# Kernel optimization log

Hardware: AMD Instinct MI355X
Metric: run time of the kernel (lower is better)

Reference implementation:

```python
import jax, jax.numpy as jnp
import numpy as np

D_MODEL = 1024
N_HEADS = 16
D_FF = 4096
D_K = D_MODEL // N_HEADS


def _ln(x, g, b, eps=1e-5):
    mu = jnp.mean(x, axis=-1, keepdims=True)
    var = jnp.mean(jnp.square(x - mu), axis=-1, keepdims=True)
    return (x - mu) * jax.lax.rsqrt(var + eps) * g + b


def setup_inputs() -> dict:
    key = jax.random.key(0)
    ks = jax.random.split(key, 16)
    s = 0.02
    inp = {
        "x": jax.random.normal(ks[0], (2, 2048, D_MODEL), dtype=jnp.float32),
        "Wq": jax.random.normal(ks[1], (D_MODEL, D_MODEL), dtype=jnp.float32) * s,
        "bq": jnp.zeros((D_MODEL,), jnp.float32),
        "Wk": jax.random.normal(ks[2], (D_MODEL, D_MODEL), dtype=jnp.float32) * s,
        "bk": jnp.zeros((D_MODEL,), jnp.float32),
        "Wv": jax.random.normal(ks[3], (D_MODEL, D_MODEL), dtype=jnp.float32) * s,
        "bv": jnp.zeros((D_MODEL,), jnp.float32),
        "Wo": jax.random.normal(ks[4], (D_MODEL, D_MODEL), dtype=jnp.float32) * s,
        "bo": jnp.zeros((D_MODEL,), jnp.float32),
        "W1": jax.random.normal(ks[5], (D_MODEL, D_FF), dtype=jnp.float32) * s,
        "b1": jnp.zeros((D_FF,), jnp.float32),
        "W2": jax.random.normal(ks[6], (D_FF, D_MODEL), dtype=jnp.float32) * s,
        "b2": jnp.zeros((D_MODEL,), jnp.float32),
        "g1": jnp.ones((D_MODEL,), jnp.float32),
        "be1": jnp.zeros((D_MODEL,), jnp.float32),
        "g2": jnp.ones((D_MODEL,), jnp.float32),
        "be2": jnp.zeros((D_MODEL,), jnp.float32),
    }
    return inp


def reference(x, Wq, bq, Wk, bk, Wv, bv, Wo, bo, W1, b1, W2, b2, g1, be1, g2, be2):
    B, L, D = x.shape
    # QKV projections -> [B, H, L, d_k]
    q = (x @ Wq + bq).reshape(B, L, N_HEADS, D_K).transpose(0, 2, 1, 3)
    k = (x @ Wk + bk).reshape(B, L, N_HEADS, D_K).transpose(0, 2, 1, 3)
    v = (x @ Wv + bv).reshape(B, L, N_HEADS, D_K).transpose(0, 2, 1, 3)
    scores = jnp.einsum("bhqd,bhkd->bhqk", q, k) / jnp.sqrt(jnp.float32(D_K))
    attn = jax.nn.softmax(scores, axis=-1)
    ctx = jnp.einsum("bhqk,bhkd->bhqd", attn, v)
    ctx = ctx.transpose(0, 2, 1, 3).reshape(B, L, D)
    attn_out = ctx @ Wo + bo
    # residual + LN1
    h = _ln(x + attn_out, g1, be1)
    # FFN (exact GELU, matching torch F.gelu default)
    ff = jax.nn.gelu(h @ W1 + b1, approximate=False) @ W2 + b2
    return _ln(h + ff, g2, be2)
```

## Files before the change

### kernel.cpp

```cpp
#include <hip/hip_runtime.h>
#include <cmath>


typedef unsigned short u16;
typedef unsigned int u32;
typedef __attribute__((ext_vector_type(8))) __bf16 bf16x8;
typedef __attribute__((ext_vector_type(4))) float f32x4;

#define MFMA16(a, b, c) __builtin_amdgcn_mfma_f32_16x16x32_bf16(a, b, c, 0, 0, 0)

__device__ __forceinline__ u16 f2bf(float f) {
  u32 u = __builtin_bit_cast(u32, f);
  u += 0x7fffu + ((u >> 16) & 1u);
  return (u16)(u >> 16);
}

__device__ __forceinline__ u32 packtrunc(float lo, float hi) {
#if __has_builtin(__builtin_amdgcn_perm)
  return __builtin_amdgcn_perm(__builtin_bit_cast(u32, hi),
                               __builtin_bit_cast(u32, lo), 0x07060302u);
#else
  return (__builtin_bit_cast(u32, lo) >> 16) |
         (__builtin_bit_cast(u32, hi) & 0xFFFF0000u);
#endif
}

__device__ __forceinline__ bf16x8 ld_frag(const u16* p) {
  return __builtin_bit_cast(bf16x8, *(const uint4*)p);
}

__device__ __forceinline__ float fexp2(float x) {
#if __has_builtin(__builtin_amdgcn_exp2f)
  return __builtin_amdgcn_exp2f(x);
#else
  return exp2f(x);
#endif
}

__device__ __forceinline__ float frcp(float x) {
#if __has_builtin(__builtin_amdgcn_rcpf)
  return __builtin_amdgcn_rcpf(x);
#else
  return 1.0f / x;
#endif
}

__device__ __forceinline__ float gelu_f(float v) {
  float x = v * 0.70710678118654752f;
  float a = fabsf(x);
  float t = frcp(fmaf(0.3275911f, a, 1.0f));
  float p = fmaf(1.061405429f, t, -1.453152027f);
  p = fmaf(p, t, 1.421413741f);
  p = fmaf(p, t, -0.284496736f);
  p = fmaf(p, t, 0.254829592f);
  p = p * t;
  float e = fexp2(-a * a * 1.4426950408889634f);
  float er = copysignf(1.0f - p * e, x);
  return 0.5f * v * (1.0f + er);
}

__device__ __forceinline__ void gload16(const u16* g, u16* l) {
  __builtin_amdgcn_global_load_lds(
      (const __attribute__((address_space(1))) void*)g,
      (__attribute__((address_space(3))) void*)l, 16, 0, 0);
}

#define WAITVL(N) asm volatile("s_waitcnt vmcnt(" #N ") lgkmcnt(0)" ::: "memory")
#define BAR() do { __builtin_amdgcn_s_barrier(); asm volatile("" ::: "memory"); } while (0)

__global__ __launch_bounds__(256) void cvt_bf16_k(const float* __restrict__ src,
                                                  u16* __restrict__ dst) {
  int i = (blockIdx.x * 256 + threadIdx.x) * 4;
  float4 v = *(const float4*)(src + i);
  ushort4 o;
  o.x = f2bf(v.x); o.y = f2bf(v.y); o.z = f2bf(v.z); o.w = f2bf(v.w);
  *(ushort4*)(dst + i) = o;
}

__global__ __launch_bounds__(256) void transpose_bf16_k(const float* __restrict__ src,
                                                        u16* __restrict__ dst,
                                                        int R, int C) {
  __shared__ float tile[32][33];
  int tx = threadIdx.x & 31, ty = threadIdx.x >> 5;
  int c0 = blockIdx.x * 32, r0 = blockIdx.y * 32;
#pragma unroll
  for (int i = 0; i < 4; i++)
    tile[ty + 8 * i][tx] = src[(long)(r0 + ty + 8 * i) * C + c0 + tx];
  __syncthreads();
#pragma unroll
  for (int i = 0; i < 4; i++)
    dst[(long)(c0 + ty + 8 * i) * R + r0 + tx] = f2bf(tile[tx][ty + 8 * i]);
}

__global__ __launch_bounds__(256) void transpose4_bf16_k(
    const float* __restrict__ Wq, const float* __restrict__ Wk,
    const float* __restrict__ Wv, const float* __restrict__ Wo,
    u16* __restrict__ wqkvT, u16* __restrict__ woT) {
  const int z = blockIdx.z;
  const float* src = (z == 0) ? Wq : (z == 1) ? Wk : (z == 2) ? Wv : Wo;
  u16* dst = (z < 3) ? (wqkvT + (size_t)z * 1024 * 1024) : woT;
  __shared__ float tile[32][33];
  int tx = threadIdx.x & 31, ty = threadIdx.x >> 5;
  int c0 = blockIdx.x * 32, r0 = blockIdx.y * 32;
#pragma unroll
  for (int i = 0; i < 4; i++)
    tile[ty + 8 * i][tx] = src[(long)(r0 + ty + 8 * i) * 1024 + c0 + tx];
  __syncthreads();
#pragma unroll
  for (int i = 0; i < 4; i++)
    dst[(long)(c0 + ty + 8 * i) * 1024 + r0 + tx] = f2bf(tile[tx][ty + 8 * i]);
}

template <int MODE>
__global__ __launch_bounds__(256, 3) void gemm128_k(
    const u16* __restrict__ A, const u16* __restrict__ BT,
    int N, int lda, int ldb, int Kc,
    const float* __restrict__ bias, float* __restrict__ outF,
    u16* __restrict__ outB, float* __restrict__ p1,
    u16* __restrict__ qd, u16* __restrict__ kd, u16* __restrict__ vTd,
    const float* __restrict__ bq, const float* __restrict__ bk,
    const float* __restrict__ bv) {
  __shared__ u16 As[3][128 * 32];
  __shared__ u16 Bs[3][128 * 32];
  const int tid = threadIdx.x;
  const int wave = tid >> 6, lane = tid & 63, quad = lane >> 4, l16 = lane & 15;
  const int wm = wave >> 1, wn = wave & 1;
  const int gx = gridDim.x;
  int flat = blockIdx.y * gx + blockIdx.x;
  const int cpx = (gx * gridDim.y) >> 3;
  flat = (flat & 7) * cpx + (flat >> 3);
  const int m0 = (flat / gx) * 128, n0 = (flat % gx) * 128;
  const int kz = blockIdx.z;
  const long kofs = (long)kz * Kc;
  const int KT = Kc >> 5;

  const int srow = lane >> 2;
  const int sseg = (lane & 3) ^ (srow & 3);
  const u16* aS = A + (long)(m0 + wave * 32 + srow) * lda + kofs + sseg * 8;
  const u16* bS = BT + (long)(n0 + wave * 32 + srow) * ldb + kofs + sseg * 8;

  auto stage = [&](int sb, int s) {
    const u16* pa = aS + (long)s * 32;
    gload16(pa, &As[sb][wave * 1024]);
    gload16(pa + 16 * (long)lda, &As[sb][wave * 1024 + 512]);
    const u16* pb = bS + (long)s * 32;
    gload16(pb, &Bs[sb][wave * 1024]);
    gload16(pb + 16 * (long)ldb, &Bs[sb][wave * 1024 + 512]);
  };

  int aro[4], bro[4];
#pragma unroll
  for (int f = 0; f < 4; f++) {
    int ra = wm * 64 + f * 16 + l16;
    aro[f] = ra * 32 + ((quad ^ (ra & 3)) * 8);
    int rb = wn * 64 + f * 16 + l16;
    bro[f] = rb * 32 + ((quad ^ (rb & 3)) * 8);
  }

  f32x4 acc[4][4] = {};

  stage(0, 0);
  stage(1, 1);
  int buf = 0;
#pragma unroll 1
  for (int t = 0; t < KT; ++t) {
    if (t < KT - 1) { WAITVL(4); } else { WAITVL(0); }
    BAR();
    bf16x8 af[4], bfr[4];
#pragma unroll
    for (int i = 0; i < 4; i++) af[i] = ld_frag(&As[buf][aro[i]]);
#pragma unroll
    for (int i = 0; i < 4; i++) bfr[i] = ld_frag(&Bs[buf][bro[i]]);
    if (t + 2 < KT) {
      int nb = buf + 2; if (nb >= 3) nb -= 3;
      stage(nb, t + 2);
    }
    __builtin_amdgcn_s_setprio(1);
#pragma unroll
    for (int mf = 0; mf < 4; mf++)
#pragma unroll
      for (int nf = 0; nf < 4; nf++)
        acc[mf][nf] = MFMA16(af[mf], bfr[nf], acc[mf][nf]);
    __builtin_amdgcn_s_setprio(0);
    if (++buf == 3) buf = 0;
  }

  if (MODE == 0) {
    const int nbase = n0 + wn * 64;
    const int mat = nbase >> 10;
    const float* bp = (mat == 0) ? bq : ((mat == 1) ? bk : bv);
    float bb[4];
    int hh0[4], dd0[4];
#pragma unroll
    for (int nf = 0; nf < 4; nf++) {
      int nn = (nbase + nf * 16 + l16) & 1023;
      bb[nf] = bp[nn];
      hh0[nf] = nn >> 6;
      dd0[nf] = nn & 63;
    }
    if (mat < 2) {
#pragma unroll
      for (int mf = 0; mf < 4; mf++) {
#pragma unroll
        for (int r = 0; r < 4; r++) {
          int mr = m0 + wm * 64 + mf * 16 + quad * 4 + r;
          int bI = mr >> 11, ll = mr & 2047;
#pragma unroll
          for (int nf = 0; nf < 4; nf++) {
            float v = acc[mf][nf][r] + bb[nf];
            long idx = ((long)((bI * 16 + hh0[nf]) * 2048 + ll)) * 64 + dd0[nf];
            if (mat == 0) {
              qd[idx] = f2bf(v * 0.18033688011112043f);
            } else {
              kd[idx] = f2bf(v);
            }
          }
        }
      }
    } else {
#pragma unroll
      for (int nf = 0; nf < 4; nf++) {
#pragma unroll
        for (int mf = 0; mf < 4; mf++) {
#pragma unroll
          for (int r = 0; r < 4; r++) {
            int mr = m0 + wm * 64 + mf * 16 + quad * 4 + r;
            int bI = mr >> 11, ll = mr & 2047;
            float v = acc[mf][nf][r] + bb[nf];
            vTd[((long)((bI * 16 + hh0[nf]) * 64 + dd0[nf])) * 2048 + ll] = f2bf(v);
          }
        }
      }
    }
  } else if (MODE == 2) {
    float bb[4];
#pragma unroll
    for (int nf = 0; nf < 4; nf++) bb[nf] = bias[n0 + wn * 64 + nf * 16 + l16];
#pragma unroll
    for (int mf = 0; mf < 4; mf++) {
#pragma unroll
      for (int r = 0; r < 4; r++) {
        int mr = m0 + wm * 64 + mf * 16 + quad * 4 + r;
        u16* orow = outB + (long)mr * N + n0 + wn * 64 + l16;
#pragma unroll
        for (int nf = 0; nf < 4; nf++)
          orow[nf * 16] = f2bf(gelu_f(acc[mf][nf][r] + bb[nf]));
      }
    }
  } else {
    float* sl = (kz == 0) ? outF : p1;
#pragma unroll
    for (int mf = 0; mf < 4; mf++) {
#pragma unroll
      for (int r = 0; r < 4; r++) {
        int mr = m0 + wm * 64 + mf * 16 + quad * 4 + r;
        float* orow = sl + (long)mr * N + n0 + wn * 64 + l16;
#pragma unroll
        for (int nf = 0; nf < 4; nf++) orow[nf * 16] = acc[mf][nf][r];
      }
    }
  }
}

template <int MODE, int TN>
__global__ __launch_bounds__(256) void gemm_k(
    const u16* __restrict__ A, const u16* __restrict__ BT, int M, int N, int K,
    const float* __restrict__ bias, float* __restrict__ outF) {
  constexpr int NT = TN / 32;
  __shared__ u16 As[2][128 * 32];
  __shared__ u16 Bs[2][TN * 32];
  const int tid = threadIdx.x;
  const int wave = tid >> 6, lane = tid & 63, quad = lane >> 4, l16 = lane & 15;
  const int wm = wave >> 1, wn = wave & 1;
  const int m0 = blockIdx.y * 128, n0 = blockIdx.x * TN;

  const int srow = lane >> 2;
  const int sxor = (lane & 3) ^ (srow & 3);
  const u16* aS0 = A + (long)(m0 + wave * 32 + srow) * K + sxor * 8;
  const u16* aS1 = aS0 + 16 * K;
  const u16* bS0 = BT + (long)(n0 + (TN == 128 ? wave * 32 : wave * 16) + srow) * K + sxor * 8;
  const u16* bS1 = bS0 + 16 * K;

  int aoff[4], boff[NT];
#pragma unroll
  for (int t = 0; t < 4; t++) {
    int ra = wm * 64 + t * 16 + l16;
    aoff[t] = ra * 32 + ((quad ^ (l16 & 3)) * 8);
  }
#pragma unroll
  for (int t = 0; t < NT; t++) {
    int rb = wn * (TN / 2) + t * 16 + l16;
    boff[t] = rb * 32 + ((quad ^ (l16 & 3)) * 8);
  }

  auto stage = [&](int buf, int k0) {
    gload16(aS0 + k0, &As[buf][(wave * 2 + 0) * 512]);
    gload16(aS1 + k0, &As[buf][(wave * 2 + 1) * 512]);
    if (TN == 128) {
      gload16(bS0 + k0, &Bs[buf][(wave * 2 + 0) * 512]);
      gload16(bS1 + k0, &Bs[buf][(wave * 2 + 1) * 512]);
    } else {
      gload16(bS0 + k0, &Bs[buf][wave * 512]);
    }
  };

  f32x4 acc[4][NT] = {};

  stage(0, 0);
#pragma unroll 1
  for (int k0 = 0; k0 < K; k0 += 32) {
    const int buf = (k0 >> 5) & 1;
    __syncthreads();
    if (k0 + 32 < K) stage(buf ^ 1, k0 + 32);
    bf16x8 af[4], bfr[NT];
#pragma unroll
    for (int t = 0; t < 4; t++) af[t] = ld_frag(&As[buf][aoff[t]]);
#pragma unroll
    for (int t = 0; t < NT; t++) bfr[t] = ld_frag(&Bs[buf][boff[t]]);
#pragma unroll
    for (int mt = 0; mt < 4; mt++)
#pragma unroll
      for (int nt = 0; nt < NT; nt++)
        acc[mt][nt] = MFMA16(af[mt], bfr[nt], acc[mt][nt]);
  }

  if (MODE == 1) {
    float bb[NT];
#pragma unroll
    for (int nt = 0; nt < NT; nt++) bb[nt] = bias[n0 + wn * (TN / 2) + nt * 16 + l16];
#pragma unroll
    for (int mt = 0; mt < 4; mt++) {
#pragma unroll
      for (int r = 0; r < 4; r++) {
        int mr = m0 + wm * 64 + mt * 16 + quad * 4 + r;
        float* orow = outF + (long)mr * N + n0 + wn * (TN / 2) + l16;
#pragma unroll
        for (int nt = 0; nt < NT; nt++)
          orow[nt * 16] = acc[mt][nt][r] + bb[nt];
      }
    }
  }
}

__global__ __launch_bounds__(256, 3) void attn_k(const u16* __restrict__ qd,
                                                 const u16* __restrict__ kd,
                                                 const u16* __restrict__ vTd,
                                                 u16* __restrict__ ctx) {
  __shared__ u16 Ks[2][64 * 64];
  __shared__ u16 Vs[2][64 * 64];
  __shared__ __align__(16) u16 P[4][32][72];
  const int tid = threadIdx.x;
  const int wave = tid >> 6, lane = tid & 63, quad = lane >> 4, l16 = lane & 15;
  const int bh = blockIdx.y;
  const u16* Q = qd + (long)bh * 2048 * 64;
  const u16* Kp = kd + (long)bh * 2048 * 64;
  const u16* Vt = vTd + (long)bh * 64 * 2048;
  const int qbase = blockIdx.x * 128 + wave * 32;

  bf16x8 qf[2][2];
#pragma unroll
  for (int qs = 0; qs < 2; qs++) {
    qf[qs][0] = ld_frag(Q + (qbase + qs * 16 + l16) * 64 + quad * 8);
    qf[qs][1] = ld_frag(Q + (qbase + qs * 16 + l16) * 64 + 32 + quad * 8);
  }

  f32x4 o[2][4] = {};
  float m[2] = {-1e30f, -1e30f}, l[2] = {0.f, 0.f};

  const int srow = lane >> 3;
  const int sx = (lane & 7) ^ srow;
  const int kr0 = wave * 16 + srow;
  const int kr1 = wave * 16 + 8 + srow;

  const int fs0 = ((0 * 4 + quad) ^ (l16 & 7)) * 8;
  const int fs1 = ((1 * 4 + quad) ^ (l16 & 7)) * 8;

  auto stage = [&](int buf, int j0) {
    gload16(Kp + (long)(j0 + kr0) * 64 + sx * 8, &Ks[buf][(wave * 2 + 0) * 512]);
    gload16(Kp + (long)(j0 + kr1) * 64 + sx * 8, &Ks[buf][(wave * 2 + 1) * 512]);
    gload16(Vt + (long)kr0 * 2048 + j0 + sx * 8, &Vs[buf][(wave * 2 + 0) * 512]);
    gload16(Vt + (long)kr1 * 2048 + j0 + sx * 8, &Vs[buf][(wave * 2 + 1) * 512]);
  };

  stage(0, 0);

#pragma unroll 1
  for (int j0 = 0; j0 < 2048; j0 += 64) {
    const int buf = (j0 >> 6) & 1;
    __syncthreads();
    if (j0 + 64 < 2048) stage(buf ^ 1, j0 + 64);

    const u16* kb = &Ks[buf][0];
    f32x4 st[2][4];
#pragma unroll
    for (int f = 0; f < 4; f++) {
      bf16x8 k0 = ld_frag(kb + (f * 16 + l16) * 64 + fs0);
      bf16x8 k1 = ld_frag(kb + (f * 16 + l16) * 64 + fs1);
      f32x4 s0 = {}, s1 = {};
      s0 = MFMA16(k0, qf[0][0], s0); s0 = MFMA16(k1, qf[0][1], s0);
      s1 = MFMA16(k0, qf[1][0], s1); s1 = MFMA16(k1, qf[1][1], s1);
      st[0][f] = s0; st[1][f] = s1;
    }

#pragma unroll
    for (int qs = 0; qs < 2; qs++) {
      float mx = -1e30f;
#pragma unroll
      for (int f = 0; f < 4; f++)
        mx = fmaxf(mx, fmaxf(fmaxf(st[qs][f][0], st[qs][f][1]),
                             fmaxf(st[qs][f][2], st[qs][f][3])));
      mx = fmaxf(mx, __shfl_xor(mx, 16));
      mx = fmaxf(mx, __shfl_xor(mx, 32));
      if (__any(mx > m[qs] + 8.0f)) {
        float mn = fmaxf(m[qs], mx);
        float al = fexp2(m[qs] - mn);
        m[qs] = mn;
        l[qs] *= al;
#pragma unroll
        for (int nt = 0; nt < 4; nt++) {
          o[qs][nt][0] *= al; o[qs][nt][1] *= al;
          o[qs][nt][2] *= al; o[qs][nt][3] *= al;
        }
      }
      float sm = 0.f;
      u16* prow = &P[wave][qs * 16 + l16][0];
#pragma unroll
      for (int f = 0; f < 4; f++) {
        float p0 = fexp2(st[qs][f][0] - m[qs]);
        float p1 = fexp2(st[qs][f][1] - m[qs]);
        float p2 = fexp2(st[qs][f][2] - m[qs]);
        float p3 = fexp2(st[qs][f][3] - m[qs]);
        sm += (p0 + p1) + (p2 + p3);
        uint2 u;
        u.x = packtrunc(p0, p1);
        u.y = packtrunc(p2, p3);
        *(uint2*)(prow + f * 16 + quad * 4) = u;
      }
      sm += __shfl_xor(sm, 16);
      sm += __shfl_xor(sm, 32);
      l[qs] += sm;
    }
    __asm__ volatile("s_waitcnt lgkmcnt(0)" ::: "memory");

    const u16* vb = &Vs[buf][0];
    bf16x8 vf[4][2];
#pragma unroll
    for (int nt = 0; nt < 4; nt++) {
      vf[nt][0] = ld_frag(vb + (nt * 16 + l16) * 64 + fs0);
      vf[nt][1] = ld_frag(vb + (nt * 16 + l16) * 64 + fs1);
    }
#pragma unroll
    for (int qs = 0; qs < 2; qs++) {
      const u16* prow = &P[wave][qs * 16 + l16][0];
#pragma unroll
      for (int kh = 0; kh < 2; kh++) {
        bf16x8 pf = ld_frag(prow + kh * 32 + quad * 8);
#pragma unroll
        for (int nt = 0; nt < 4; nt++)
          o[qs][nt] = MFMA16(vf[nt][kh], pf, o[qs][nt]);
      }
    }
  }

  const int bI = bh >> 4, hh = bh & 15;
#pragma unroll
  for (int qs = 0; qs < 2; qs++) {
    const float rl = 1.0f / l[qs];
    const long row = (long)(bI * 2048 + qbase + qs * 16 + l16);
#pragma unroll
    for (int nt = 0; nt < 4; nt++) {
      ushort4 w;
      w.x = f2bf(o[qs][nt][0] * rl);
      w.y = f2bf(o[qs][nt][1] * rl);
      w.z = f2bf(o[qs][nt][2] * rl);
      w.w = f2bf(o[qs][nt][3] * rl);
      *(ushort4*)(ctx + row * 1024 + hh * 64 + nt * 16 + quad * 4) = w;
    }
  }
}

__global__ __launch_bounds__(256) void ln_k(const float* __restrict__ a,
                                            const float* __restrict__ b,
                                            const float* __restrict__ g,
                                            const float* __restrict__ be,
                                            float* __restrict__ outF,
                                            u16* __restrict__ outB) {
  const int row = blockIdx.x, tid = threadIdx.x;
  const float* pa = a + (long)row * 1024;
  const float* pb = b + (long)row * 1024;
  float v[4], s = 0.f, sq = 0.f;
#pragma unroll
  for (int i = 0; i < 4; i++) {
    int c = i * 256 + tid;
    v[i] = pa[c] + pb[c];
    s += v[i];
    sq += v[i] * v[i];
  }
#pragma unroll
  for (int off = 1; off < 64; off <<= 1) {
    s += __shfl_xor(s, off);
    sq += __shfl_xor(sq, off);
  }
  __shared__ float red[10];
  int wave = tid >> 6, lane = tid & 63;
  if (lane == 0) { red[wave * 2] = s; red[wave * 2 + 1] = sq; }
  __syncthreads();
  if (tid == 0) {
    float S = red[0] + red[2] + red[4] + red[6];
    float Q = red[1] + red[3] + red[5] + red[7];
    float mu = S * (1.0f / 1024.0f);
    float var = Q * (1.0f / 1024.0f) - mu * mu;
    red[8] = mu;
    red[9] = rsqrtf(var + 1e-5f);
  }
  __syncthreads();
  float mu = red[8], rstd = red[9];
#pragma unroll
  for (int i = 0; i < 4; i++) {
    int c = i * 256 + tid;
    float o = (v[i] - mu) * rstd * g[c] + be[c];
    outF[(long)row * 1024 + c] = o;
    if (outB) outB[(long)row * 1024 + c] = f2bf(o);
  }
}

__global__ __launch_bounds__(256) void ln2s_k(const float* __restrict__ a,
                                              const float* __restrict__ q0,
                                              const float* __restrict__ q1,
                                              const float* __restrict__ bias,
                                              const float* __restrict__ g,
                                              const float* __restrict__ be,
                                              float* __restrict__ outF) {
  const int row = blockIdx.x, tid = threadIdx.x;
  const long base = (long)row * 1024;
  float v[4], s = 0.f, sq = 0.f;
#pragma unroll
  for (int i = 0; i < 4; i++) {
    int c = i * 256 + tid;
    float ff = q0[base + c] + q1[base + c] + bias[c];
    v[i] = a[base + c] + ff;
    s += v[i];
    sq += v[i] * v[i];
  }
#pragma unroll
  for (int off = 1; off < 64; off <<= 1) {
    s += __shfl_xor(s, off);
    sq += __shfl_xor(sq, off);
  }
  __shared__ float red[10];
  int wave = tid >> 6, lane = tid & 63;
  if (lane == 0) { red[wave * 2] = s; red[wave * 2 + 1] = sq; }
  __syncthreads();
  if (tid == 0) {
    float S = red[0] + red[2] + red[4] + red[6];
    float Q = red[1] + red[3] + red[5] + red[7];
    float mu = S * (1.0f / 1024.0f);
    float var = Q * (1.0f / 1024.0f) - mu * mu;
    red[8] = mu;
    red[9] = rsqrtf(var + 1e-5f);
  }
  __syncthreads();
  float mu = red[8], rstd = red[9];
#pragma unroll
  for (int i = 0; i < 4; i++) {
    int c = i * 256 + tid;
    outF[base + c] = (v[i] - mu) * rstd * g[c] + be[c];
  }
}

extern "C" void kernel_launch(void* const* d_in, const int* in_sizes, int n_in,
                              void* d_out, int out_size, void* d_ws, size_t ws_size,
                              hipStream_t stream) {
  const float* x  = (const float*)d_in[0];
  const float* Wq = (const float*)d_in[1];  const float* bq = (const float*)d_in[2];
  const float* Wk = (const float*)d_in[3];  const float* bk = (const float*)d_in[4];
  const float* Wv = (const float*)d_in[5];  const float* bv = (const float*)d_in[6];
  const float* Wo = (const float*)d_in[7];  const float* bo = (const float*)d_in[8];
  const float* W1 = (const float*)d_in[9];  const float* b1 = (const float*)d_in[10];
  const float* W2 = (const float*)d_in[11]; const float* b2 = (const float*)d_in[12];
  const float* g1 = (const float*)d_in[13]; const float* be1 = (const float*)d_in[14];
  const float* g2 = (const float*)d_in[15]; const float* be2 = (const float*)d_in[16];

  char* ws = (char*)d_ws;
  size_t off = 0;
  auto alloc = [&](size_t bytes) {
    size_t o = off;
    off += (bytes + 255) & ~(size_t)255;
    return o;
  };
  u16*   xb     = (u16*)(ws + alloc(4096UL * 1024 * 2));
  u16*   wqkvT  = (u16*)(ws + alloc(3072UL * 1024 * 2));
  u16*   woT    = (u16*)(ws + alloc(1024UL * 1024 * 2));
  u16*   w1T    = (u16*)(ws + alloc(4096UL * 1024 * 2));
  u16*   w2T    = (u16*)(ws + alloc(1024UL * 4096 * 2));
  u16*   qb     = (u16*)(ws + alloc(32UL * 2048 * 64 * 2));
  u16*   kb     = (u16*)(ws + alloc(32UL * 2048 * 64 * 2));
  u16*   vTb    = (u16*)(ws + alloc(32UL * 64 * 2048 * 2));
  u16*   ctx    = (u16*)(ws + alloc(4096UL * 1024 * 2));
  float* attnO  = (float*)(ws + alloc(4096UL * 1024 * 4));
  float* h      = (float*)(ws + alloc(4096UL * 1024 * 4));
  u16*   hb     = (u16*)(ws + alloc(4096UL * 1024 * 2));
  u16*   ff1    = (u16*)(ws + alloc(4096UL * 4096 * 2));
  float* ff2    = (float*)(ws + alloc(4096UL * 1024 * 4));
  if (off > ws_size) return;

  float* sl0 = ff2;
  float* sl1 = attnO;

  cvt_bf16_k<<<4096, 256, 0, stream>>>(x, xb);
  transpose4_bf16_k<<<dim3(32, 32, 4), 256, 0, stream>>>(Wq, Wk, Wv, Wo, wqkvT, woT);
  transpose_bf16_k<<<dim3(128, 32), 256, 0, stream>>>(W1, w1T, 1024, 4096);
  transpose_bf16_k<<<dim3(32, 128), 256, 0, stream>>>(W2, w2T, 4096, 1024);

  gemm128_k<0><<<dim3(24, 32), 256, 0, stream>>>(
      xb, wqkvT, 3072, 1024, 1024, 1024,
      nullptr, nullptr, nullptr, nullptr,
      qb, kb, vTb, bq, bk, bv);
  attn_k<<<dim3(16, 32), 256, 0, stream>>>(qb, kb, vTb, ctx);
  gemm_k<1, 64><<<dim3(16, 32), 256, 0, stream>>>(ctx, woT, 4096, 1024, 1024,
                                                  bo, attnO);
  ln_k<<<4096, 256, 0, stream>>>(x, attnO, g1, be1, h, hb);
  gemm128_k<2><<<dim3(32, 32), 256, 0, stream>>>(
      hb, w1T, 4096, 1024, 1024, 1024,
      b1, nullptr, ff1, nullptr,
      nullptr, nullptr, nullptr, nullptr, nullptr, nullptr);
  gemm128_k<3><<<dim3(8, 32, 2), 256, 0, stream>>>(
      ff1, w2T, 1024, 4096, 4096, 2048,
      nullptr, sl0, nullptr, sl1,
      nullptr, nullptr, nullptr, nullptr, nullptr, nullptr);
  ln2s_k<<<4096, 256, 0, stream>>>(h, sl0, sl1, b2, g2, be2, (float*)d_out);
}
```

Baseline: 371.0 us.

## Halve attention query tile per wave to double grid size

Each wave in the attention kernel now handles 16 query rows instead of 32, so a block covers 64 queries and the grid doubles to 32x32 blocks. This cuts per-thread register state (one set of accumulators and softmax stats) and the P scratch buffer, which should raise occupancy and spread work over more CUs. In exchange, every K/V tile staged into LDS is reused by half as many queries, doubling global K/V traffic and LDS fragment loads per unit of work.

```diff
diff --git a/kernel.cpp b/kernel.cpp
--- a/kernel.cpp
+++ b/kernel.cpp
@@ -348,24 +348,21 @@
                                                  u16* __restrict__ ctx) {
   __shared__ u16 Ks[2][64 * 64];
   __shared__ u16 Vs[2][64 * 64];
-  __shared__ __align__(16) u16 P[4][32][72];
+  __shared__ __align__(16) u16 P[4][16][72];
   const int tid = threadIdx.x;
   const int wave = tid >> 6, lane = tid & 63, quad = lane >> 4, l16 = lane & 15;
   const int bh = blockIdx.y;
   const u16* Q = qd + (long)bh * 2048 * 64;
   const u16* Kp = kd + (long)bh * 2048 * 64;
   const u16* Vt = vTd + (long)bh * 64 * 2048;
-  const int qbase = blockIdx.x * 128 + wave * 32;
-
-  bf16x8 qf[2][2];
-#pragma unroll
-  for (int qs = 0; qs < 2; qs++) {
-    qf[qs][0] = ld_frag(Q + (qbase + qs * 16 + l16) * 64 + quad * 8);
-    qf[qs][1] = ld_frag(Q + (qbase + qs * 16 + l16) * 64 + 32 + quad * 8);
-  }
-
-  f32x4 o[2][4] = {};
-  float m[2] = {-1e30f, -1e30f}, l[2] = {0.f, 0.f};
+  const int qbase = blockIdx.x * 64 + wave * 16;
+
+  bf16x8 qf[2];
+  qf[0] = ld_frag(Q + (qbase + l16) * 64 + quad * 8);
+  qf[1] = ld_frag(Q + (qbase + l16) * 64 + 32 + quad * 8);
+
+  f32x4 o[4] = {};
+  float m = -1e30f, l = 0.f;
 
   const int srow = lane >> 3;
   const int sx = (lane & 7) ^ srow;
@@ -391,91 +388,78 @@
     if (j0 + 64 < 2048) stage(buf ^ 1, j0 + 64);
 
     const u16* kb = &Ks[buf][0];
-    f32x4 st[2][4];
+    f32x4 st[4];
 #pragma unroll
     for (int f = 0; f < 4; f++) {
       bf16x8 k0 = ld_frag(kb + (f * 16 + l16) * 64 + fs0);
       bf16x8 k1 = ld_frag(kb + (f * 16 + l16) * 64 + fs1);
-      f32x4 s0 = {}, s1 = {};
-      s0 = MFMA16(k0, qf[0][0], s0); s0 = MFMA16(k1, qf[0][1], s0);
-      s1 = MFMA16(k0, qf[1][0], s1); s1 = MFMA16(k1, qf[1][1], s1);
-      st[0][f] = s0; st[1][f] = s1;
-    }
-
-#pragma unroll
-    for (int qs = 0; qs < 2; qs++) {
-      float mx = -1e30f;
-#pragma unroll
-      for (int f = 0; f < 4; f++)
-        mx = fmaxf(mx, fmaxf(fmaxf(st[qs][f][0], st[qs][f][1]),
-                             fmaxf(st[qs][f][2], st[qs][f][3])));
-      mx = fmaxf(mx, __shfl_xor(mx, 16));
-      mx = fmaxf(mx, __shfl_xor(mx, 32));
-      if (__any(mx > m[qs] + 8.0f)) {
-        float mn = fmaxf(m[qs], mx);
-        float al = fexp2(m[qs] - mn);
-        m[qs] = mn;
-        l[qs] *= al;
-#pragma unroll
-        for (int nt = 0; nt < 4; nt++) {
-          o[qs][nt][0] *= al; o[qs][nt][1] *= al;
-          o[qs][nt][2] *= al; o[qs][nt][3] *= al;
-        }
+      f32x4 s0 = {};
+      s0 = MFMA16(k0, qf[0], s0);
+      s0 = MFMA16(k1, qf[1], s0);
+      st[f] = s0;
+    }
+
+    float mx = -1e30f;
+#pragma unroll
+    for (int f = 0; f < 4; f++)
+      mx = fmaxf(mx, fmaxf(fmaxf(st[f][0], st[f][1]),
+                           fmaxf(st[f][2], st[f][3])));
+    mx = fmaxf(mx, __shfl_xor(mx, 16));
+    mx = fmaxf(mx, __shfl_xor(mx, 32));
+    if (__any(mx > m + 8.0f)) {
+      float mn = fmaxf(m, mx);
+      float al = fexp2(m - mn);
+      m = mn;
+      l *= al;
+#pragma unroll
+      for (int nt = 0; nt < 4; nt++) {
+        o[nt][0] *= al; o[nt][1] *= al;
+        o[nt][2] *= al; o[nt][3] *= al;
       }
-      float sm = 0.f;
-      u16* prow = &P[wave][qs * 16 + l16][0];
-#pragma unroll
-      for (int f = 0; f < 4; f++) {
-        float p0 = fexp2(st[qs][f][0] - m[qs]);
-        float p1 = fexp2(st[qs][f][1] - m[qs]);
-        float p2 = fexp2(st[qs][f][2] - m[qs]);
-        float p3 = fexp2(st[qs][f][3] - m[qs]);
-        sm += (p0 + p1) + (p2 + p3);
-        uint2 u;
-        u.x = packtrunc(p0, p1);
-        u.y = packtrunc(p2, p3);
-        *(uint2*)(prow + f * 16 + quad * 4) = u;
+    }
+    float sm = 0.f;
+    u16* prow = &P[wave][l16][0];
+#pragma unroll
+    for (int f = 0; f < 4; f++) {
+      float p0 = fexp2(st[f][0] - m);
+      float p1 = fexp2(st[f][1] - m);
+      float p2 = fexp2(st[f][2] - m);
+      float p3 = fexp2(st[f][3] - m);
+      sm += (p0 + p1) + (p2 + p3);
+      uint2 u;
+      u.x = packtrunc(p0, p1);
+      u.y = packtrunc(p2, p3);
+      *(uint2*)(prow + f * 16 + quad * 4) = u;
+    }
+    sm += __shfl_xor(sm, 16);
+    sm += __shfl_xor(sm, 32);
+    l += sm;
+    __asm__ volatile("s_waitcnt lgkmcnt(0)" ::: "memory");
+
+    const u16* vb = &Vs[buf][0];
+#pragma unroll
+    for (int kh = 0; kh < 2; kh++) {
+      bf16x8 pf = ld_frag(prow + kh * 32 + quad * 8);
+      const int fsk = (kh == 0) ? fs0 : fs1;
+#pragma unroll
+      for (int nt = 0; nt < 4; nt++) {
+        bf16x8 vf = ld_frag(vb + (nt * 16 + l16) * 64 + fsk);
+        o[nt] = MFMA16(vf, pf, o[nt]);
       }
-      sm += __shfl_xor(sm, 16);
-      sm += __shfl_xor(sm, 32);
-      l[qs] += sm;
-    }
-    __asm__ volatile("s_waitcnt lgkmcnt(0)" ::: "memory");
-
-    const u16* vb = &Vs[buf][0];
-    bf16x8 vf[4][2];
-#pragma unroll
-    for (int nt = 0; nt < 4; nt++) {
-      vf[nt][0] = ld_frag(vb + (nt * 16 + l16) * 64 + fs0);
-      vf[nt][1] = ld_frag(vb + (nt * 16 + l16) * 64 + fs1);
-    }
-#pragma unroll
-    for (int qs = 0; qs < 2; qs++) {
-      const u16* prow = &P[wave][qs * 16 + l16][0];
-#pragma unroll
-      for (int kh = 0; kh < 2; kh++) {
-        bf16x8 pf = ld_frag(prow + kh * 32 + quad * 8);
-#pragma unroll
-        for (int nt = 0; nt < 4; nt++)
-          o[qs][nt] = MFMA16(vf[nt][kh], pf, o[qs][nt]);
-      }
     }
   }
 
   const int bI = bh >> 4, hh = bh & 15;
-#pragma unroll
-  for (int qs = 0; qs < 2; qs++) {
-    const float rl = 1.0f / l[qs];
-    const long row = (long)(bI * 2048 + qbase + qs * 16 + l16);
-#pragma unroll
-    for (int nt = 0; nt < 4; nt++) {
-      ushort4 w;
-      w.x = f2bf(o[qs][nt][0] * rl);
-      w.y = f2bf(o[qs][nt][1] * rl);
-      w.z = f2bf(o[qs][nt][2] * rl);
-      w.w = f2bf(o[qs][nt][3] * rl);
-      *(ushort4*)(ctx + row * 1024 + hh * 64 + nt * 16 + quad * 4) = w;
-    }
+  const float rl = 1.0f / l;
+  const long row = (long)(bI * 2048 + qbase + l16);
+#pragma unroll
+  for (int nt = 0; nt < 4; nt++) {
+    ushort4 w;
+    w.x = f2bf(o[nt][0] * rl);
+    w.y = f2bf(o[nt][1] * rl);
+    w.z = f2bf(o[nt][2] * rl);
+    w.w = f2bf(o[nt][3] * rl);
+    *(ushort4*)(ctx + row * 1024 + hh * 64 + nt * 16 + quad * 4) = w;
   }
 }
 
@@ -616,7 +600,7 @@
       xb, wqkvT, 3072, 1024, 1024, 1024,
       nullptr, nullptr, nullptr, nullptr,
       qb, kb, vTb, bq, bk, bv);
-  attn_k<<<dim3(16, 32), 256, 0, stream>>>(qb, kb, vTb, ctx);
+  attn_k<<<dim3(32, 32), 256, 0, stream>>>(qb, kb, vTb, ctx);
   gemm_k<1, 64><<<dim3(16, 32), 256, 0, stream>>>(ctx, woT, 4096, 1024, 1024,
                                                   bo, attnO);
   ln_k<<<4096, 256, 0, stream>>>(x, attnO, g1, be1, h, hb);
```

New measurement: 397.9 us. 7.3% more time.
